# Performance work log

Measured on AMD Instinct MI355X. Metric: run time of the kernel, lower is better.

The kernel has to match this reference:

```python
import jax, jax.numpy as jnp
import numpy as np

RHO = 1.0
MU = 1e-05
DT = 1.0 / 32
DX = 1.0 / 255
DY = 1.0 / 255


def _residuals(x, std):
    # x: [B, 3, H, W]; torch does x *= std (pure version here)
    x = x * std
    u = x[:, 0]  # [B, H, W]
    v = x[:, 1]
    p = x[:, 2]
    r = jnp.roll

    dudt = (r(u, -1, 0) - r(u, 1, 0)) / DT
    dvdt = (r(v, -1, 0) - r(v, 1, 0)) / DT
    dudx = (r(u, -1, 1) - r(u, 1, 1)) / (2 * DX)
    dudy = (r(u, -1, 2) - r(u, 1, 2)) / (2 * DY)
    dvdx = (r(v, -1, 1) - r(v, 1, 1)) / (2 * DX)
    dvdy = (r(v, -1, 2) - r(v, 1, 2)) / (2 * DY)
    dpdx = (r(p, -1, 1) - r(p, 1, 1)) / (2 * DX)
    dpdy = (r(p, -1, 2) - r(p, 1, 2)) / (2 * DY)
    d2udx2 = (r(u, -1, 1) - 2 * u + r(u, 1, 1)) / DX ** 2
    d2udy2 = (r(u, -1, 2) - 2 * u + r(u, 1, 2)) / DY ** 2
    d2vdx2 = (r(v, -1, 1) - 2 * v + r(v, 1, 1)) / DX ** 2
    d2vdy2 = (r(v, -1, 2) - 2 * v + r(v, 1, 2)) / DY ** 2

    t = lambda a: a[1:-1, 1:-1, 1:-1]  # trim periodic-wrap halo
    u, v = t(u), t(v)
    r0 = jnp.abs(t(dudx) + t(dvdy))
    r1 = jnp.abs(RHO * (t(dudt) + u * t(dudx) + v * t(dudy)) + t(dpdx)
                 - MU * (t(d2udx2) + t(d2udy2)))
    r2 = jnp.abs(RHO * (t(dvdt) + u * t(dvdx) + v * t(dvdy)) + t(dpdy)
                 - MU * (t(d2vdx2) + t(d2vdy2)))
    return r0, r1, r2


def setup_inputs() -> dict:
    key = jax.random.key(0)
    k1, k2, k3 = jax.random.split(key, 3)
    B, C, H, W = 64, 3, 512, 512
    x = jax.random.normal(k1, (B, C, H, W), dtype=jnp.float32)
    y = jax.random.normal(k2, (B, C, H, W), dtype=jnp.float32)
    std = jax.random.uniform(k3, (), dtype=jnp.float32)
    return {"x": x, "y": y, "std": std}


def reference(x, y, std):
    r0_y, r1_y, r2_y = _residuals(y, std)
    r0_x, r1_x, r2_x = _residuals(x, std)
    d0 = jnp.mean((r0_y - r0_x) ** 2)
    d1 = jnp.mean((r1_y - r1_x) ** 2)
    d2 = jnp.mean((r2_y - r2_x) ** 2)
    return 0.001 * (d0 + d1 + d2)
```

## Files before the change

kernel.cpp:

```cpp
#include <hip/hip_runtime.h>


constexpr int Wd   = 512;
constexpr int CSTR = 512 * 512;
constexpr int BSTR = 3 * 512 * 512;

__device__ __forceinline__ float4 ld4(const float* p) {
    return *reinterpret_cast<const float4*>(p);
}
__device__ __forceinline__ float4 scale4(float4 a, float s) {
    return make_float4(a.x * s, a.y * s, a.z * s, a.w * s);
}

__device__ __forceinline__ void plane_resid(
    const float (&L)[3][4][512],
    int io, int jt, int j0,
    float4 eu, float4 ev, float4 ep,
    float4 mu, float4 cu, float4 nus,
    float4 mv, float4 cv, float4 nvs,
    float4 cp, float sdx,
    float r0[4], float r1[4], float r2[4])
{
    float4 uxm, vxm, pxm, uxp, vxp, pxp;
    if (io == 0) { uxm = eu; vxm = ev; pxm = ep; }
    else {
        uxm = ld4(&L[0][io - 1][j0]);
        vxm = ld4(&L[1][io - 1][j0]);
        pxm = ld4(&L[2][io - 1][j0]);
    }
    if (io == 3) { uxp = eu; vxp = ev; pxp = ep; }
    else {
        uxp = ld4(&L[0][io + 1][j0]);
        vxp = ld4(&L[1][io + 1][j0]);
        pxp = ld4(&L[2][io + 1][j0]);
    }

    float u_l = __shfl_up(cu.w, 1);
    float v_l = __shfl_up(cv.w, 1);
    float p_l = __shfl_up(cp.w, 1);
    float u_r = __shfl_down(cu.x, 1);
    float v_r = __shfl_down(cv.x, 1);
    float p_r = __shfl_down(cp.x, 1);
    const int lane = jt & 63;
    if (lane == 0) {
        const int jm = (j0 == 0) ? 0 : (j0 - 1);
        u_l = L[0][io][jm]; v_l = L[1][io][jm]; p_l = L[2][io][jm];
    }
    if (lane == 63) {
        const int jp = (j0 >= 508) ? 511 : (j0 + 4);
        u_r = L[0][io][jp]; v_r = L[1][io][jp]; p_r = L[2][io][jp];
    }

    const float ucA[4] = {cu.x, cu.y, cu.z, cu.w};
    const float vcA[4] = {cv.x, cv.y, cv.z, cv.w};
    const float umA[4] = {mu.x, mu.y, mu.z, mu.w};
    const float vmA[4] = {mv.x, mv.y, mv.z, mv.w};
    const float unA[4] = {nus.x, nus.y, nus.z, nus.w};
    const float vnA[4] = {nvs.x, nvs.y, nvs.z, nvs.w};
    const float ul[4]  = {u_l, cu.x, cu.y, cu.z};
    const float ur[4]  = {cu.y, cu.z, cu.w, u_r};
    const float vl[4]  = {v_l, cv.x, cv.y, cv.z};
    const float vr[4]  = {cv.y, cv.z, cv.w, v_r};
    const float pl[4]  = {p_l, cp.x, cp.y, cp.z};
    const float pr[4]  = {cp.y, cp.z, cp.w, p_r};
    const float uxpA[4] = {uxp.x, uxp.y, uxp.z, uxp.w};
    const float uxmA[4] = {uxm.x, uxm.y, uxm.z, uxm.w};
    const float vxpA[4] = {vxp.x, vxp.y, vxp.z, vxp.w};
    const float vxmA[4] = {vxm.x, vxm.y, vxm.z, vxm.w};
    const float pxpA[4] = {pxp.x, pxp.y, pxp.z, pxp.w};
    const float pxmA[4] = {pxm.x, pxm.y, pxm.z, pxm.w};

    #pragma unroll
    for (int k = 0; k < 4; ++k) {
        const float dudx = (uxpA[k] - uxmA[k]) * 127.5f;
        const float dvdx = (vxpA[k] - vxmA[k]) * 127.5f;
        const float dpdx = (pxpA[k] - pxmA[k]) * sdx;
        const float dudy = (ur[k] - ul[k]) * 127.5f;
        const float dvdy = (vr[k] - vl[k]) * 127.5f;
        const float dpdy = (pr[k] - pl[k]) * sdx;
        const float lapu = (uxpA[k] + uxmA[k] + ur[k] + ul[k]) * 0.65025f
                         - 2.601f * ucA[k];
        const float lapv = (vxpA[k] + vxmA[k] + vr[k] + vl[k]) * 0.65025f
                         - 2.601f * vcA[k];
        r0[k] = fabsf(dudx + dvdy);
        r1[k] = fabsf((unA[k] - umA[k]) * 32.0f + ucA[k] * dudx + vcA[k] * dudy
                      + dpdx - lapu);
        r2[k] = fabsf((vnA[k] - vmA[k]) * 32.0f + ucA[k] * dvdx + vcA[k] * dvdy
                      + dpdy - lapv);
    }
}

__global__ __launch_bounds__(512)
void ns_loss_kernel(const float* __restrict__ X, const float* __restrict__ Y,
                    const float* __restrict__ stdp, double* __restrict__ acc)
{
    __shared__ float lds[2][3][4][512];
    __shared__ float smr[3][8];

    const float s   = *stdp;
    const float sdx = s * 127.5f;

    const int orig = blockIdx.x;
    const int wg   = (orig & 7) * 64 + (orig >> 3);
    const int z    = wg >> 7;
    const int band = wg & 127;

    const int tid = threadIdx.x;
    const int jt  = tid & 127;
    const int io  = tid >> 7;
    const int j0  = jt << 2;
    const int irow = 1 + band * 4 + io;
    const int i    = min(irow, 511);
    const bool vrow = (irow <= 510);
    const int bs = 1 + 15 * z + (z == 3 ? 1 : 0);
    const int nsteps = (z < 2) ? 15 : 16;

    int c = bs * BSTR + i * Wd + j0;
    const int cup  = (i < 511) ? Wd : 0;
    const int eoff = (io == 0) ? -Wd : cup;
    const bool isedge = (io == 0) || (io == 3);

    float4 xmu = scale4(ld4(X + c - BSTR), s);
    float4 xcu = scale4(ld4(X + c), s);
    float4 xmv = scale4(ld4(X + c - BSTR + CSTR), s);
    float4 xcv = scale4(ld4(X + c + CSTR), s);
    float4 ymu = scale4(ld4(Y + c - BSTR), s);
    float4 ycu = scale4(ld4(Y + c), s);
    float4 ymv = scale4(ld4(Y + c - BSTR + CSTR), s);
    float4 ycv = scale4(ld4(Y + c + CSTR), s);
    float4 xnu = ld4(X + c + BSTR);
    float4 xnv = ld4(X + c + BSTR + CSTR);
    float4 xcp = ld4(X + c + 2 * CSTR);
    float4 ynu = ld4(Y + c + BSTR);
    float4 ynv = ld4(Y + c + BSTR + CSTR);
    float4 ycp = ld4(Y + c + 2 * CSTR);
    float4 xeu = make_float4(0,0,0,0), xev = xeu, xep = xeu;
    float4 yeu = xeu, yev = xeu, yep = xeu;
    if (isedge) {
        xeu = scale4(ld4(X + c + eoff), s);
        xev = scale4(ld4(X + c + CSTR + eoff), s);
        xep = ld4(X + c + 2 * CSTR + eoff);
        yeu = scale4(ld4(Y + c + eoff), s);
        yev = scale4(ld4(Y + c + CSTR + eoff), s);
        yep = ld4(Y + c + 2 * CSTR + eoff);
    }

    float s0 = 0.0f, s1 = 0.0f, s2 = 0.0f;

    for (int it = 0; it < nsteps; ++it) {
        const int cn = c + ((it + 1 < nsteps) ? BSTR : 0);

        *(float4*)&lds[0][0][io][j0] = xcu;
        *(float4*)&lds[0][1][io][j0] = xcv;
        *(float4*)&lds[0][2][io][j0] = xcp;
        *(float4*)&lds[1][0][io][j0] = ycu;
        *(float4*)&lds[1][1][io][j0] = ycv;
        *(float4*)&lds[1][2][io][j0] = ycp;
        asm volatile("s_waitcnt lgkmcnt(0)" ::: "memory");
        __builtin_amdgcn_s_barrier();

        const float4 xnus = scale4(xnu, s), xnvs = scale4(xnv, s);
        const float4 ynus = scale4(ynu, s), ynvs = scale4(ynv, s);
        xnu = ld4(X + cn + BSTR);
        xnv = ld4(X + cn + BSTR + CSTR);
        ynu = ld4(Y + cn + BSTR);
        ynv = ld4(Y + cn + BSTR + CSTR);
        float4 xcp2 = ld4(X + cn + 2 * CSTR);
        float4 ycp2 = ld4(Y + cn + 2 * CSTR);
        float4 xeu2 = xeu, xev2 = xev, xep2 = xep;
        float4 yeu2 = yeu, yev2 = yev, yep2 = yep;
        if (isedge) {
            xeu2 = scale4(ld4(X + cn + eoff), s);
            xev2 = scale4(ld4(X + cn + CSTR + eoff), s);
            xep2 = ld4(X + cn + 2 * CSTR + eoff);
            yeu2 = scale4(ld4(Y + cn + eoff), s);
            yev2 = scale4(ld4(Y + cn + CSTR + eoff), s);
            yep2 = ld4(Y + cn + 2 * CSTR + eoff);
        }

        float r0x[4], r1x[4], r2x[4], r0y[4], r1y[4], r2y[4];
        plane_resid(lds[0], io, jt, j0, xeu, xev, xep,
                    xmu, xcu, xnus, xmv, xcv, xnvs, xcp, sdx, r0x, r1x, r2x);
        plane_resid(lds[1], io, jt, j0, yeu, yev, yep,
                    ymu, ycu, ynus, ymv, ycv, ynvs, ycp, sdx, r0y, r1y, r2y);

        #pragma unroll
        for (int k = 0; k < 4; ++k) {
            float e0 = r0y[k] - r0x[k];
            float e1 = r1y[k] - r1x[k];
            float e2 = r2y[k] - r2x[k];
            const bool dead = (!vrow) || (k == 0 && j0 == 0)
                                      || (k == 3 && j0 == 508);
            if (dead) { e0 = 0.0f; e1 = 0.0f; e2 = 0.0f; }
            s0 += e0 * e0; s1 += e1 * e1; s2 += e2 * e2;
        }

        xmu = xcu; xcu = xnus; xmv = xcv; xcv = xnvs;
        ymu = ycu; ycu = ynus; ymv = ycv; ycv = ynvs;
        xcp = xcp2; ycp = ycp2;
        xeu = xeu2; xev = xev2; xep = xep2;
        yeu = yeu2; yev = yev2; yep = yep2;
        asm volatile("s_waitcnt lgkmcnt(0)" ::: "memory");
        __builtin_amdgcn_s_barrier();
        c = cn;
    }

    for (int o = 32; o > 0; o >>= 1) {
        s0 += __shfl_down(s0, o);
        s1 += __shfl_down(s1, o);
        s2 += __shfl_down(s2, o);
    }
    const int wid = tid >> 6, lane = tid & 63;
    if (lane == 0) { smr[0][wid] = s0; smr[1][wid] = s1; smr[2][wid] = s2; }
    __syncthreads();
    if (tid == 0) {
        double t0 = 0, t1 = 0, t2 = 0;
        #pragma unroll
        for (int w = 0; w < 8; ++w) {
            t0 += (double)smr[0][w];
            t1 += (double)smr[1][w];
            t2 += (double)smr[2][w];
        }
        atomicAdd(&acc[0], t0);
        atomicAdd(&acc[1], t1);
        atomicAdd(&acc[2], t2);
    }
}

__global__ void ns_finalize_kernel(const double* __restrict__ acc,
                                   float* __restrict__ out)
{
    if (threadIdx.x == 0) {
        const double N = 62.0 * 510.0 * 510.0;
        out[0] = (float)(1.0e-3 * (acc[0] + acc[1] + acc[2]) / N);
    }
}

extern "C" void kernel_launch(void* const* d_in, const int* in_sizes, int n_in,
                              void* d_out, int out_size, void* d_ws, size_t ws_size,
                              hipStream_t stream) {
    const float* X    = (const float*)d_in[0];
    const float* Y    = (const float*)d_in[1];
    const float* stdp = (const float*)d_in[2];
    float* out  = (float*)d_out;
    double* acc = (double*)d_ws;

    hipMemsetAsync(acc, 0, 3 * sizeof(double), stream);

    dim3 block(512);
    dim3 grid(512);
    ns_loss_kernel<<<grid, block, 0, stream>>>(X, Y, stdp, acc);
    ns_finalize_kernel<<<1, 64, 0, stream>>>(acc, out);
}
```

Measured before the change: 124.3 us.

## Split each row band into two column halves with 256-thread blocks

Halves the block width so each workgroup covers 256 columns of a 4-row band, doubling the grid to 1024 blocks of 256 threads. Because a half-row no longer spans the full width, the left and right halo columns are loaded from global memory by the edge lanes and double-buffered across the time loop, replacing the previous LDS lookups at wave boundaries. The aim is more and smaller workgroups for better occupancy and load balance, at the cost of extra scalar halo loads and more atomics.

```diff
diff --git a/kernel.cpp b/kernel.cpp
--- a/kernel.cpp
+++ b/kernel.cpp
@@ -13,26 +13,29 @@
 }
 
 __device__ __forceinline__ void plane_resid(
-    const float (&L)[3][4][512],
-    int io, int jt, int j0,
+    const float (&L)[3][4][256],
+    int io, int jt, int jl,
     float4 eu, float4 ev, float4 ep,
     float4 mu, float4 cu, float4 nus,
     float4 mv, float4 cv, float4 nvs,
-    float4 cp, float sdx,
+    float4 cp,
+    float uL, float vL, float pL,
+    float uR, float vR, float pR,
+    float sdx,
     float r0[4], float r1[4], float r2[4])
 {
     float4 uxm, vxm, pxm, uxp, vxp, pxp;
     if (io == 0) { uxm = eu; vxm = ev; pxm = ep; }
     else {
-        uxm = ld4(&L[0][io - 1][j0]);
-        vxm = ld4(&L[1][io - 1][j0]);
-        pxm = ld4(&L[2][io - 1][j0]);
+        uxm = ld4(&L[0][io - 1][jl]);
+        vxm = ld4(&L[1][io - 1][jl]);
+        pxm = ld4(&L[2][io - 1][jl]);
     }
     if (io == 3) { uxp = eu; vxp = ev; pxp = ep; }
     else {
-        uxp = ld4(&L[0][io + 1][j0]);
-        vxp = ld4(&L[1][io + 1][j0]);
-        pxp = ld4(&L[2][io + 1][j0]);
+        uxp = ld4(&L[0][io + 1][jl]);
+        vxp = ld4(&L[1][io + 1][jl]);
+        pxp = ld4(&L[2][io + 1][jl]);
     }
 
     float u_l = __shfl_up(cu.w, 1);
@@ -41,15 +44,8 @@
     float u_r = __shfl_down(cu.x, 1);
     float v_r = __shfl_down(cv.x, 1);
     float p_r = __shfl_down(cp.x, 1);
-    const int lane = jt & 63;
-    if (lane == 0) {
-        const int jm = (j0 == 0) ? 0 : (j0 - 1);
-        u_l = L[0][io][jm]; v_l = L[1][io][jm]; p_l = L[2][io][jm];
-    }
-    if (lane == 63) {
-        const int jp = (j0 >= 508) ? 511 : (j0 + 4);
-        u_r = L[0][io][jp]; v_r = L[1][io][jp]; p_r = L[2][io][jp];
-    }
+    if (jt == 0)  { u_l = uL; v_l = vL; p_l = pL; }
+    if (jt == 63) { u_r = uR; v_r = vR; p_r = pR; }
 
     const float ucA[4] = {cu.x, cu.y, cu.z, cu.w};
     const float vcA[4] = {cv.x, cv.y, cv.z, cv.w};
@@ -90,35 +86,40 @@
     }
 }
 
-__global__ __launch_bounds__(512)
+__global__ __launch_bounds__(256)
 void ns_loss_kernel(const float* __restrict__ X, const float* __restrict__ Y,
                     const float* __restrict__ stdp, double* __restrict__ acc)
 {
-    __shared__ float lds[2][3][4][512];
-    __shared__ float smr[3][8];
+    __shared__ float lds[2][3][4][256];
+    __shared__ float smr[3][4];
 
     const float s   = *stdp;
     const float sdx = s * 127.5f;
 
     const int orig = blockIdx.x;
-    const int wg   = (orig & 7) * 64 + (orig >> 3);
-    const int z    = wg >> 7;
-    const int band = wg & 127;
+    const int wg   = (orig & 7) * 128 + (orig >> 3);
+    const int z    = wg >> 8;
+    const int rem  = wg & 255;
+    const int jh   = rem >> 7;
+    const int band = rem & 127;
 
     const int tid = threadIdx.x;
-    const int jt  = tid & 127;
-    const int io  = tid >> 7;
-    const int j0  = jt << 2;
+    const int io  = tid >> 6;
+    const int jt  = tid & 63;
+    const int jl  = jt << 2;
+    const int j0g = (jh << 8) + jl;
     const int irow = 1 + band * 4 + io;
     const int i    = min(irow, 511);
     const bool vrow = (irow <= 510);
     const int bs = 1 + 15 * z + (z == 3 ? 1 : 0);
     const int nsteps = (z < 2) ? 15 : 16;
 
-    int c = bs * BSTR + i * Wd + j0;
+    int c = bs * BSTR + i * Wd + j0g;
     const int cup  = (i < 511) ? Wd : 0;
     const int eoff = (io == 0) ? -Wd : cup;
     const bool isedge = (io == 0) || (io == 3);
+    const int offL = (j0g == 0) ? 0 : -1;
+    const int offR = (j0g == 508) ? 3 : 4;
 
     float4 xmu = scale4(ld4(X + c - BSTR), s);
     float4 xcu = scale4(ld4(X + c), s);
@@ -144,18 +145,32 @@
         yev = scale4(ld4(Y + c + CSTR + eoff), s);
         yep = ld4(Y + c + 2 * CSTR + eoff);
     }
+    float xul = 0, xvl = 0, xpl = 0, yul = 0, yvl = 0, ypl = 0;
+    float xur = 0, xvr = 0, xpr = 0, yur = 0, yvr = 0, ypr = 0;
+    if (jt == 0) {
+        xul = X[c + offL] * s; xvl = X[c + CSTR + offL] * s;
+        xpl = X[c + 2 * CSTR + offL];
+        yul = Y[c + offL] * s; yvl = Y[c + CSTR + offL] * s;
+        ypl = Y[c + 2 * CSTR + offL];
+    }
+    if (jt == 63) {
+        xur = X[c + offR] * s; xvr = X[c + CSTR + offR] * s;
+        xpr = X[c + 2 * CSTR + offR];
+        yur = Y[c + offR] * s; yvr = Y[c + CSTR + offR] * s;
+        ypr = Y[c + 2 * CSTR + offR];
+    }
 
     float s0 = 0.0f, s1 = 0.0f, s2 = 0.0f;
 
     for (int it = 0; it < nsteps; ++it) {
         const int cn = c + ((it + 1 < nsteps) ? BSTR : 0);
 
-        *(float4*)&lds[0][0][io][j0] = xcu;
-        *(float4*)&lds[0][1][io][j0] = xcv;
-        *(float4*)&lds[0][2][io][j0] = xcp;
-        *(float4*)&lds[1][0][io][j0] = ycu;
-        *(float4*)&lds[1][1][io][j0] = ycv;
-        *(float4*)&lds[1][2][io][j0] = ycp;
+        *(float4*)&lds[0][0][io][jl] = xcu;
+        *(float4*)&lds[0][1][io][jl] = xcv;
+        *(float4*)&lds[0][2][io][jl] = xcp;
+        *(float4*)&lds[1][0][io][jl] = ycu;
+        *(float4*)&lds[1][1][io][jl] = ycv;
+        *(float4*)&lds[1][2][io][jl] = ycp;
         asm volatile("s_waitcnt lgkmcnt(0)" ::: "memory");
         __builtin_amdgcn_s_barrier();
 
@@ -177,20 +192,38 @@
             yev2 = scale4(ld4(Y + cn + CSTR + eoff), s);
             yep2 = ld4(Y + cn + 2 * CSTR + eoff);
         }
+        float xul2 = xul, xvl2 = xvl, xpl2 = xpl;
+        float yul2 = yul, yvl2 = yvl, ypl2 = ypl;
+        float xur2 = xur, xvr2 = xvr, xpr2 = xpr;
+        float yur2 = yur, yvr2 = yvr, ypr2 = ypr;
+        if (jt == 0) {
+            xul2 = X[cn + offL] * s; xvl2 = X[cn + CSTR + offL] * s;
+            xpl2 = X[cn + 2 * CSTR + offL];
+            yul2 = Y[cn + offL] * s; yvl2 = Y[cn + CSTR + offL] * s;
+            ypl2 = Y[cn + 2 * CSTR + offL];
+        }
+        if (jt == 63) {
+            xur2 = X[cn + offR] * s; xvr2 = X[cn + CSTR + offR] * s;
+            xpr2 = X[cn + 2 * CSTR + offR];
+            yur2 = Y[cn + offR] * s; yvr2 = Y[cn + CSTR + offR] * s;
+            ypr2 = Y[cn + 2 * CSTR + offR];
+        }
 
         float r0x[4], r1x[4], r2x[4], r0y[4], r1y[4], r2y[4];
-        plane_resid(lds[0], io, jt, j0, xeu, xev, xep,
-                    xmu, xcu, xnus, xmv, xcv, xnvs, xcp, sdx, r0x, r1x, r2x);
-        plane_resid(lds[1], io, jt, j0, yeu, yev, yep,
-                    ymu, ycu, ynus, ymv, ycv, ynvs, ycp, sdx, r0y, r1y, r2y);
+        plane_resid(lds[0], io, jt, jl, xeu, xev, xep,
+                    xmu, xcu, xnus, xmv, xcv, xnvs, xcp,
+                    xul, xvl, xpl, xur, xvr, xpr, sdx, r0x, r1x, r2x);
+        plane_resid(lds[1], io, jt, jl, yeu, yev, yep,
+                    ymu, ycu, ynus, ymv, ycv, ynvs, ycp,
+                    yul, yvl, ypl, yur, yvr, ypr, sdx, r0y, r1y, r2y);
 
         #pragma unroll
         for (int k = 0; k < 4; ++k) {
             float e0 = r0y[k] - r0x[k];
             float e1 = r1y[k] - r1x[k];
             float e2 = r2y[k] - r2x[k];
-            const bool dead = (!vrow) || (k == 0 && j0 == 0)
-                                      || (k == 3 && j0 == 508);
+            const bool dead = (!vrow) || (k == 0 && j0g == 0)
+                                      || (k == 3 && j0g == 508);
             if (dead) { e0 = 0.0f; e1 = 0.0f; e2 = 0.0f; }
             s0 += e0 * e0; s1 += e1 * e1; s2 += e2 * e2;
         }
@@ -200,6 +233,10 @@
         xcp = xcp2; ycp = ycp2;
         xeu = xeu2; xev = xev2; xep = xep2;
         yeu = yeu2; yev = yev2; yep = yep2;
+        xul = xul2; xvl = xvl2; xpl = xpl2;
+        yul = yul2; yvl = yvl2; ypl = ypl2;
+        xur = xur2; xvr = xvr2; xpr = xpr2;
+        yur = yur2; yvr = yvr2; ypr = ypr2;
         asm volatile("s_waitcnt lgkmcnt(0)" ::: "memory");
         __builtin_amdgcn_s_barrier();
         c = cn;
@@ -210,20 +247,16 @@
         s1 += __shfl_down(s1, o);
         s2 += __shfl_down(s2, o);
     }
-    const int wid = tid >> 6, lane = tid & 63;
-    if (lane == 0) { smr[0][wid] = s0; smr[1][wid] = s1; smr[2][wid] = s2; }
+    const int wid = tid >> 6;
+    if (jt == 0) { smr[0][wid] = s0; smr[1][wid] = s1; smr[2][wid] = s2; }
     __syncthreads();
     if (tid == 0) {
-        double t0 = 0, t1 = 0, t2 = 0;
-        #pragma unroll
-        for (int w = 0; w < 8; ++w) {
-            t0 += (double)smr[0][w];
-            t1 += (double)smr[1][w];
-            t2 += (double)smr[2][w];
-        }
-        atomicAdd(&acc[0], t0);
-        atomicAdd(&acc[1], t1);
-        atomicAdd(&acc[2], t2);
+        atomicAdd(&acc[0], (double)smr[0][0] + (double)smr[0][1]
+                         + (double)smr[0][2] + (double)smr[0][3]);
+        atomicAdd(&acc[1], (double)smr[1][0] + (double)smr[1][1]
+                         + (double)smr[1][2] + (double)smr[1][3]);
+        atomicAdd(&acc[2], (double)smr[2][0] + (double)smr[2][1]
+                         + (double)smr[2][2] + (double)smr[2][3]);
     }
 }
 
@@ -247,8 +280,8 @@
 
     hipMemsetAsync(acc, 0, 3 * sizeof(double), stream);
 
-    dim3 block(512);
-    dim3 grid(512);
+    dim3 block(256);
+    dim3 grid(1024);
     ns_loss_kernel<<<grid, block, 0, stream>>>(X, Y, stdp, acc);
     ns_finalize_kernel<<<1, 64, 0, stream>>>(acc, out);
 }
```

After: 147.0 us. +18.3%, slower.
